# Kernel optimization log

Measured on AMD Instinct MI355X. Metric: run time of the kernel, lower is better.

## Reference

```python
import jax, jax.numpy as jnp
import numpy as np

EPS = 1e-5  # BatchNorm1d eps (eval mode: running_mean=0, running_var=1)

def _bn(h, gamma, beta):
    return h * (gamma / jnp.sqrt(1.0 + EPS)) + beta

def _edgeconv(x, src, dst, W, b, gamma, beta, n_nodes):
    # PyG EdgeConv: message = nn(concat[x_i, x_j - x_i]), aggr='max' at target i
    xi = x[dst]            # [E, D] target features
    xj = x[src]            # [E, D] source features
    m = jnp.concatenate([xi, xj - xi], axis=-1)  # [E, 2D]
    m = _bn(m @ W + b, gamma, beta)              # per-edge Linear + BN
    h = jax.ops.segment_max(m, dst, num_segments=n_nodes)
    # PyG fills nodes with no incoming edges with 0 for max aggregation
    return jnp.where(jnp.isneginf(h), 0.0, h)

def _mean_pool(h, batch, n_graphs):
    s = jax.ops.segment_sum(h, batch, num_segments=n_graphs)
    cnt = jax.ops.segment_sum(jnp.ones((h.shape[0],), h.dtype), batch, num_segments=n_graphs)
    return s / jnp.maximum(cnt, 1.0)[:, None]

def setup_inputs() -> dict:
    key = jax.random.key(0)
    ks = jax.random.split(key, 12)
    N, E, D, G = 65536, 131072, 1024, 64
    x = jax.random.normal(ks[0], (N, D), dtype=jnp.float32)
    edge_index = jax.random.randint(ks[1], (2, E), 0, N, dtype=jnp.int64)
    batch = jnp.sort(jax.random.randint(ks[2], (N,), 0, G, dtype=jnp.int64))
    sc = 1.0 / np.sqrt(D)
    sc2 = 1.0 / np.sqrt(2 * D)
    W0 = jax.random.uniform(ks[3], (D, D), jnp.float32, -sc, sc)
    b0 = jnp.zeros((D,), jnp.float32)
    g0 = jnp.ones((D,), jnp.float32); be0 = jnp.zeros((D,), jnp.float32)
    W1 = jax.random.uniform(ks[4], (2 * D, D), jnp.float32, -sc2, sc2)
    b1 = jnp.zeros((D,), jnp.float32)
    g1 = jnp.ones((D,), jnp.float32); be1 = jnp.zeros((D,), jnp.float32)
    W2 = jax.random.uniform(ks[5], (2 * D, D), jnp.float32, -sc2, sc2)
    b2 = jnp.zeros((D,), jnp.float32)
    g2 = jnp.ones((D,), jnp.float32); be2 = jnp.zeros((D,), jnp.float32)
    Wr = jax.random.uniform(ks[6], (D, 2), jnp.float32, -sc, sc)
    br = jnp.zeros((2,), jnp.float32)
    return dict(x=x, edge_index=edge_index, batch=batch,
                W0=W0, b0=b0, g0=g0, be0=be0,
                W1=W1, b1=b1, g1=g1, be1=be1,
                W2=W2, b2=b2, g2=g2, be2=be2,
                Wr=Wr, br=br)

def reference(x, edge_index, batch, W0, b0, g0, be0, W1, b1, g1, be1, W2, b2, g2, be2, Wr, br):
    N = x.shape[0]
    G = 64
    src, dst = edge_index[0], edge_index[1]
    # Block 0: node-wise Linear+BN, then mean pool (dropout is identity in eval)
    h0 = _bn(x @ W0 + b0, g0, be0)
    p0 = _mean_pool(h0, batch, G)
    # Blocks 1,2: EdgeConv (gather-concat-MLP-scatterMax), then mean pool
    h1 = _edgeconv(x, src, dst, W1, b1, g1, be1, N)
    p1 = _mean_pool(h1, batch, G)
    h2 = _edgeconv(x, src, dst, W2, b2, g2, be2, N)
    p2 = _mean_pool(h2, batch, G)
    acc = p0 + p1 + p2
    return acc @ Wr + br  # [G, 2]
```

## Files before the change

### kernel.cpp

```cpp
#include <hip/hip_runtime.h>
#include <stdint.h>

#define DD   1024
#define GNUM 64

typedef __attribute__((ext_vector_type(8))) short short8;
typedef __attribute__((ext_vector_type(4))) float f32x4;

__device__ __forceinline__ ushort f2bf(float f) {
    unsigned u = __float_as_uint(f);
    u += 0x7FFFu + ((u >> 16) & 1u);
    return (ushort)(u >> 16);
}
__device__ __forceinline__ float bf2f(ushort h) {
    return __uint_as_float(((unsigned)h) << 16);
}

__device__ __forceinline__ void load_lds16(const void* g, void* l) {
    __builtin_amdgcn_global_load_lds(
        (const __attribute__((address_space(1))) unsigned*)(uintptr_t)g,
        (__attribute__((address_space(3))) unsigned*)(uint32_t)(uintptr_t)l,
        16, 0, 0);
}

__device__ __forceinline__ int lbound(const int* a, int n, int v) {
    int lo = 0, hi = n;
    while (lo < hi) { int m = (lo + hi) >> 1; if (a[m] < v) lo = m + 1; else hi = m; }
    return lo;
}

__global__ __launch_bounds__(256) void zero_kernel(int* __restrict__ p, int n) {
    int i = blockIdx.x * 256 + threadIdx.x;
    if (i < n) p[i] = 0;
}

__global__ __launch_bounds__(256) void degflag_kernel(
    const int* __restrict__ ei, int* __restrict__ deg,
    int* __restrict__ flag, int E)
{
    int e = blockIdx.x * 256 + threadIdx.x;
    if (e < E) {
        atomicAdd(&deg[ei[E + e]], 1);
        flag[ei[e]] = 1;
    }
}

__global__ __launch_bounds__(256) void scanA_kernel(
    const int* __restrict__ deg, const int* __restrict__ flag,
    int* __restrict__ ld, int* __restrict__ lf,
    int* __restrict__ bd, int* __restrict__ bf)
{
    __shared__ int sd[256], sf[256];
    const int b = blockIdx.x, t = threadIdx.x;
    const int i = b * 256 + t;
    const int d = deg[i], f = flag[i];
    sd[t] = d; sf[t] = f;
    __syncthreads();
    for (int ofs = 1; ofs < 256; ofs <<= 1) {
        int vd = (t >= ofs) ? sd[t - ofs] : 0;
        int vf = (t >= ofs) ? sf[t - ofs] : 0;
        __syncthreads();
        sd[t] += vd; sf[t] += vf;
        __syncthreads();
    }
    ld[i] = sd[t] - d;
    lf[i] = sf[t] - f;
    if (t == 255) { bd[b] = sd[255]; bf[b] = sf[255]; }
}

__global__ __launch_bounds__(256) void scanB_kernel(
    const int* __restrict__ bd, const int* __restrict__ bf,
    int* __restrict__ od, int* __restrict__ of_, int* __restrict__ nsrc)
{
    __shared__ int sd[256], sf[256];
    const int t = threadIdx.x;
    const int d = bd[t], f = bf[t];
    sd[t] = d; sf[t] = f;
    __syncthreads();
    for (int ofs = 1; ofs < 256; ofs <<= 1) {
        int vd = (t >= ofs) ? sd[t - ofs] : 0;
        int vf = (t >= ofs) ? sf[t - ofs] : 0;
        __syncthreads();
        sd[t] += vd; sf[t] += vf;
        __syncthreads();
    }
    od[t] = sd[t] - d;
    of_[t] = sf[t] - f;
    if (t == 255) *nsrc = sf[255];
}

__global__ __launch_bounds__(256) void scanC_kernel(
    const int* __restrict__ flag, const int* __restrict__ ld,
    const int* __restrict__ lf, const int* __restrict__ od,
    const int* __restrict__ of_, int* __restrict__ rowptr,
    int* __restrict__ cursor, int* __restrict__ rank,
    int* __restrict__ perm, int N, int E)
{
    const int b = blockIdx.x, t = threadIdx.x;
    const int i = b * 256 + t;
    const int rd = od[b] + ld[i];
    rowptr[i] = rd;
    cursor[i] = rd;
    const int rf = of_[b] + lf[i];
    rank[i] = rf;
    if (flag[i]) perm[rf] = i;
    if (i == N - 1) rowptr[N] = E;
}

__global__ __launch_bounds__(256) void scatter_kernel(
    const int* __restrict__ ei, int* __restrict__ cursor,
    const int* __restrict__ rank, int* __restrict__ col, int E)
{
    int e = blockIdx.x * 256 + threadIdx.x;
    if (e < E) {
        int d = ei[E + e];
        int pos = atomicAdd(&cursor[d], 1);
        col[pos] = rank[ei[e]];
    }
}

__global__ __launch_bounds__(256) void cvtmean_kernel(
    const float* __restrict__ x, const int* __restrict__ batch,
    const int* __restrict__ deg, ushort* __restrict__ xh,
    float* __restrict__ pm, float* __restrict__ pp, int N)
{
    const int b = blockIdx.x;
    const int g = b >> 5, sub = b & 31;
    const int d4 = threadIdx.x * 4;

    const int glo = lbound(batch, N, g);
    const int ghi = lbound(batch, N, g + 1);
    const int len = ghi - glo;
    const int s0 = glo + (len * sub) / 32;
    const int s1 = glo + (len * (sub + 1)) / 32;

    float4 sum = make_float4(0.f, 0.f, 0.f, 0.f);
    float4 sump = make_float4(0.f, 0.f, 0.f, 0.f);
    for (int r = s0; r < s1; ++r) {
        float4 v = *(const float4*)(x + (size_t)r * 1024 + d4);
        sum.x += v.x; sum.y += v.y; sum.z += v.z; sum.w += v.w;
        if (deg[r] > 0) { sump.x += v.x; sump.y += v.y; sump.z += v.z; sump.w += v.w; }
        ushort4 h = make_ushort4(f2bf(v.x), f2bf(v.y), f2bf(v.z), f2bf(v.w));
        *(ushort4*)(xh + (size_t)r * 1024 + d4) = h;
    }
    size_t o = (size_t)(g * 32 + sub) * 1024 + d4;
    *(float4*)(pm + o) = sum;
    *(float4*)(pp + o) = sump;
}

__global__ __launch_bounds__(256) void xbar2_kernel(
    const float* __restrict__ pm, const float* __restrict__ pp,
    const int* __restrict__ batch, float* __restrict__ Xbar,
    float* __restrict__ xsp, int N)
{
    int g = blockIdx.x >> 2;
    int c = ((blockIdx.x & 3) << 8) + threadIdx.x;
    float s = 0.f, sp = 0.f;
    #pragma unroll
    for (int k = 0; k < 32; ++k) {
        s  += pm[(size_t)(g * 32 + k) * 1024 + c];
        sp += pp[(size_t)(g * 32 + k) * 1024 + c];
    }
    int cnt = lbound(batch, N, g + 1) - lbound(batch, N, g);
    if (cnt < 1) cnt = 1;
    Xbar[g * 1024 + c] = s / (float)cnt;
    xsp[g * 1024 + c] = sp;
}

__global__ __launch_bounds__(256) void npos_kernel(
    const int* __restrict__ deg, const int* __restrict__ batch,
    float* __restrict__ npos, int N)
{
    __shared__ int r[256];
    int g = blockIdx.x, t = threadIdx.x;
    int glo = lbound(batch, N, g);
    int ghi = lbound(batch, N, g + 1);
    int c = 0;
    for (int i = glo + t; i < ghi; i += 256) c += (deg[i] > 0) ? 1 : 0;
    r[t] = c;
    __syncthreads();
    for (int s = 128; s > 0; s >>= 1) {
        if (t < s) r[t] += r[t + s];
        __syncthreads();
    }
    if (t == 0) npos[g] = (float)r[0];
}

__global__ __launch_bounds__(256) void wbig_kernel(
    const float* __restrict__ W1, const float* __restrict__ W2,
    const float* __restrict__ g1, const float* __restrict__ g2,
    ushort* __restrict__ Wt)
{
    __shared__ float tile[32][33];
    const float SF = 1.0f / sqrtf(1.0f + 1e-5f);
    int k0 = blockIdx.x * 32, c0 = blockIdx.y * 32;
    int tx = threadIdx.x & 31, ty = threadIdx.x >> 5;
    int sec = c0 >> 10;
    int cl = (c0 & 1023) + tx;
    const float* W  = sec ? W2 : W1;
    const float* gv = sec ? g2 : g1;
    float sc = gv[cl] * SF;
    #pragma unroll
    for (int j = 0; j < 4; ++j) {
        int k = k0 + ty + j * 8;
        tile[ty + j * 8][tx] = W[(size_t)(k + 1024) * 1024 + cl] * sc;
    }
    __syncthreads();
    #pragma unroll
    for (int j = 0; j < 4; ++j) {
        int cc = ty + j * 8;
        Wt[(size_t)(c0 + cc) * 1024 + k0 + tx] = f2bf(tile[tx][cc]);
    }
}

__global__ __launch_bounds__(256) void wfold_kernel(
    const float* __restrict__ W0, const float* __restrict__ g0,
    const float* __restrict__ Wr, float* __restrict__ Wfold)
{
    __shared__ float r0s[256], r1s[256];
    const float SF = 1.0f / sqrtf(1.0f + 1e-5f);
    int k = blockIdx.x, t = threadIdx.x;
    float a0 = 0.f, a1 = 0.f;
    for (int c = t; c < 1024; c += 256) {
        float w = W0[(size_t)k * 1024 + c] * (g0[c] * SF);
        a0 += w * Wr[c * 2];
        a1 += w * Wr[c * 2 + 1];
    }
    r0s[t] = a0; r1s[t] = a1;
    __syncthreads();
    for (int s = 128; s > 0; s >>= 1) {
        if (t < s) { r0s[t] += r0s[t + s]; r1s[t] += r1s[t + s]; }
        __syncthreads();
    }
    if (t == 0) { Wfold[k * 2] = r0s[0]; Wfold[k * 2 + 1] = r1s[0]; }
}

__global__ __launch_bounds__(256) void wufold_kernel(
    const float* __restrict__ W1, const float* __restrict__ W2,
    const float* __restrict__ g1, const float* __restrict__ g2,
    const float* __restrict__ Wr, float* __restrict__ Wufold)
{
    __shared__ float r0s[256], r1s[256];
    const float SF = 1.0f / sqrtf(1.0f + 1e-5f);
    int k = blockIdx.x, t = threadIdx.x;
    float a0 = 0.f, a1 = 0.f;
    for (int c = t; c < 1024; c += 256) {
        float wu = (W1[(size_t)k * 1024 + c] - W1[(size_t)(k + 1024) * 1024 + c]) * (g1[c] * SF)
                 + (W2[(size_t)k * 1024 + c] - W2[(size_t)(k + 1024) * 1024 + c]) * (g2[c] * SF);
        a0 += wu * Wr[c * 2];
        a1 += wu * Wr[c * 2 + 1];
    }
    r0s[t] = a0; r1s[t] = a1;
    __syncthreads();
    for (int s = 128; s > 0; s >>= 1) {
        if (t < s) { r0s[t] += r0s[t + s]; r1s[t] += r1s[t + s]; }
        __syncthreads();
    }
    if (t == 0) { Wufold[k * 2] = r0s[0]; Wufold[k * 2 + 1] = r1s[0]; }
}

__global__ __launch_bounds__(256) void bfold_kernel(
    const float* __restrict__ b1, const float* __restrict__ g1, const float* __restrict__ be1,
    const float* __restrict__ b2, const float* __restrict__ g2, const float* __restrict__ be2,
    const float* __restrict__ Wr, float* __restrict__ bUWr)
{
    __shared__ float r0s[256], r1s[256];
    const float SF = 1.0f / sqrtf(1.0f + 1e-5f);
    int t = threadIdx.x;
    float a0 = 0.f, a1 = 0.f;
    for (int c = t; c < 1024; c += 256) {
        float bu = b1[c] * (g1[c] * SF) + be1[c] + b2[c] * (g2[c] * SF) + be2[c];
        a0 += bu * Wr[c * 2];
        a1 += bu * Wr[c * 2 + 1];
    }
    r0s[t] = a0; r1s[t] = a1;
    __syncthreads();
    for (int s = 128; s > 0; s >>= 1) {
        if (t < s) { r0s[t] += r0s[t + s]; r1s[t] += r1s[t + s]; }
        __syncthreads();
    }
    if (t == 0) { bUWr[0] = r0s[0]; bUWr[1] = r1s[0]; }
}

__global__ __launch_bounds__(512, 2) void gemm8_kernel(
    const ushort* __restrict__ A, const ushort* __restrict__ Bt,
    const int* __restrict__ perm, const int* __restrict__ nsrc,
    ushort* __restrict__ C)
{
    __shared__ __align__(16) ushort SM[65536];
    const int tid  = threadIdx.x;
    const int w    = tid >> 6;
    const int lane = tid & 63;
    const int wr = w >> 2;
    const int wc = w & 3;

    const int bx  = blockIdx.x;
    const int cx  = bx & 7;
    const int idx = bx >> 3;
    const int mt  = (idx >> 3) * 8 + cx;
    const int nt  = idx & 7;
    const int m0 = mt * 256;
    const int n0 = nt * 256;

    const int nsv = *nsrc;
    if (m0 >= nsv) return;

    const int srow = lane >> 3;
    const int csw  = ((lane & 7) ^ srow) << 3;

    const int prow = w * 8 + srow;
    int pr[4];
    #pragma unroll
    for (int z = 0; z < 4; ++z) {
        int r = m0 + z * 64 + prow;
        int p_ = perm[r];
        pr[z] = (r < nsv) ? p_ : 0;
    }

    auto stA = [&](int t, int h) {
        if (t >= 16) return;
        const int c = t & 1;
        const ushort* s0 = A + (size_t)pr[2 * h]     * 1024 + t * 64 + csw;
        const ushort* s1 = A + (size_t)pr[2 * h + 1] * 1024 + t * 64 + csw;
        ushort* d = SM + c * 16384 + h * 8192 + w * 512;
        load_lds16(s0, d);
        load_lds16(s1, d + 4096);
    };
    auto stB = [&](int t, int h) {
        if (t >= 16) return;
        const int c = t & 1;
        const ushort* s = Bt + (size_t)(n0 + h * 128 + w * 8 + srow) * 1024 + t * 64 + csw;
        ushort* d = SM + 32768 + c * 16384 + h * 8192 + w * 512;
        load_lds16(s, d);
        load_lds16(s + (size_t)64 * 1024, d + 4096);
    };

    const int cbk0 = ((lane >> 4) << 4);
    const int cbx2 = (lane & 7) << 4;
    auto rdA = [&](int c, int i, int kk) -> short8 {
        int row = i * 16 + (lane & 15);
        int cb  = (kk * 64 + cbk0) ^ cbx2;
        return *(const short8*)((const char*)SM + (c * 16384 + wr * 8192) * 2 + row * 128 + cb);
    };
    auto rdB = [&](int c, int j, int kk) -> short8 {
        int row = (wc & 1) * 64 + j * 16 + (lane & 15);
        int cb  = (kk * 64 + cbk0) ^ cbx2;
        return *(const short8*)((const char*)SM + 65536 + (c * 16384 + (wc >> 1) * 8192) * 2 + row * 128 + cb);
    };

    f32x4 acc[8][4];
    #pragma unroll
    for (int i = 0; i < 8; ++i)
        #pragma unroll
        for (int j = 0; j < 4; ++j)
            acc[i][j] = (f32x4){0.f, 0.f, 0.f, 0.f};

    short8 afr[4][2], bfr[4][2];

    stA(0, 0); stA(0, 1); stB(0, 0); stB(0, 1); stB(1, 0); stB(1, 1);
    asm volatile("s_waitcnt vmcnt(4)" ::: "memory");
    __builtin_amdgcn_s_barrier();

    for (int t = 0; t < 16; ++t) {
        const int c = t & 1;
        #pragma unroll
        for (int i = 0; i < 4; ++i) { afr[i][0] = rdA(c, i, 0); afr[i][1] = rdA(c, i, 1); }
        #pragma unroll
        for (int j = 0; j < 2; ++j) { bfr[j][0] = rdB(c, j, 0); bfr[j][1] = rdB(c, j, 1); }
        stA(t + 1, 0);
        __builtin_amdgcn_s_barrier();
        __builtin_amdgcn_s_setprio(1);
        #pragma unroll
        for (int i = 0; i < 4; ++i)
            #pragma unroll
            for (int j = 0; j < 2; ++j) {
                acc[i][j] = __builtin_amdgcn_mfma_f32_16x16x32_bf16(bfr[j][0], afr[i][0], acc[i][j], 0, 0, 0);
                acc[i][j] = __builtin_amdgcn_mfma_f32_16x16x32_bf16(bfr[j][1], afr[i][1], acc[i][j], 0, 0, 0);
            }
        __builtin_amdgcn_s_setprio(0);
        __builtin_amdgcn_s_barrier();

        #pragma unroll
        for (int j = 2; j < 4; ++j) { bfr[j][0] = rdB(c, j, 0); bfr[j][1] = rdB(c, j, 1); }
        stA(t + 1, 1);
        __builtin_amdgcn_s_barrier();
        __builtin_amdgcn_s_setprio(1);
        #pragma unroll
        for (int i = 0; i < 4; ++i)
            #pragma unroll
            for (int j = 2; j < 4; ++j) {
                acc[i][j] = __builtin_amdgcn_mfma_f32_16x16x32_bf16(bfr[j][0], afr[i][0], acc[i][j], 0, 0, 0);
                acc[i][j] = __builtin_amdgcn_mfma_f32_16x16x32_bf16(bfr[j][1], afr[i][1], acc[i][j], 0, 0, 0);
            }
        __builtin_amdgcn_s_setprio(0);
        __builtin_amdgcn_s_barrier();

        #pragma unroll
        for (int i = 0; i < 4; ++i) { afr[i][0] = rdA(c, i + 4, 0); afr[i][1] = rdA(c, i + 4, 1); }
        stB(t + 2, 0);
        __builtin_amdgcn_s_barrier();
        __builtin_amdgcn_s_setprio(1);
        #pragma unroll
        for (int i = 0; i < 4; ++i)
            #pragma unroll
            for (int j = 2; j < 4; ++j) {
                acc[i + 4][j] = __builtin_amdgcn_mfma_f32_16x16x32_bf16(bfr[j][0], afr[i][0], acc[i + 4][j], 0, 0, 0);
                acc[i + 4][j] = __builtin_amdgcn_mfma_f32_16x16x32_bf16(bfr[j][1], afr[i][1], acc[i + 4][j], 0, 0, 0);
            }
        __builtin_amdgcn_s_setprio(0);
        __builtin_amdgcn_s_barrier();

        stB(t + 2, 1);
        __builtin_amdgcn_s_barrier();
        __builtin_amdgcn_s_setprio(1);
        #pragma unroll
        for (int i = 0; i < 4; ++i)
            #pragma unroll
            for (int j = 0; j < 2; ++j) {
                acc[i + 4][j] = __builtin_amdgcn_mfma_f32_16x16x32_bf16(bfr[j][0], afr[i][0], acc[i + 4][j], 0, 0, 0);
                acc[i + 4][j] = __builtin_amdgcn_mfma_f32_16x16x32_bf16(bfr[j][1], afr[i][1], acc[i + 4][j], 0, 0, 0);
            }
        __builtin_amdgcn_s_setprio(0);
        if (t < 15) {
            if (t < 14) asm volatile("s_waitcnt vmcnt(4)" ::: "memory");
            else        asm volatile("s_waitcnt vmcnt(0)" ::: "memory");
            __builtin_amdgcn_s_barrier();
        }
    }

    __syncthreads();
    {
        const int mls = wr * 128 + (lane & 15);
        const int nls = wc * 64 + ((lane >> 4) << 2);
        #pragma unroll
        for (int j = 0; j < 4; ++j) {
            const int nl = nls + j * 16;
            #pragma unroll
            for (int i = 0; i < 8; ++i) {
                const int ml = mls + i * 16;
                unsigned lo = (unsigned)f2bf(acc[i][j][0]) |
                              ((unsigned)f2bf(acc[i][j][1]) << 16);
                unsigned hi = (unsigned)f2bf(acc[i][j][2]) |
                              ((unsigned)f2bf(acc[i][j][3]) << 16);
                int u = (ml * 256 + nl) ^ ((ml & 15) << 2);
                *(uint2*)(SM + u) = make_uint2(lo, hi);
            }
        }
    }
    __syncthreads();
    #pragma unroll
    for (int p = 0; p < 32; ++p) {
        const int idx2 = p * 512 + tid;
        const int row = idx2 >> 6;
        const int cu  = (idx2 & 63) * 4;
        int u = (row * 256 + cu) ^ ((row & 15) << 2);
        uint2 v = *(const uint2*)(SM + u);
        *(uint2*)(&C[(size_t)(m0 + row) * 2048 + n0 + cu]) = v;
    }
}

__global__ __launch_bounds__(256) void edgepool_kernel(
    const ushort* __restrict__ C, const int* __restrict__ rowptr,
    const int* __restrict__ colb, const int* __restrict__ batch,
    float* __restrict__ partial, int N)
{
    const int b = blockIdx.x;
    const int g = b >> 4, sub = b & 15;
    const int d8 = threadIdx.x * 8;

    const int glo = lbound(batch, N, g);
    const int ghi = lbound(batch, N, g + 1);
    const int len = ghi - glo;
    const int s0 = glo + (len * sub) / 16;
    const int s1 = glo + (len * (sub + 1)) / 16;

    float vsum[8];
    #pragma unroll
    for (int q = 0; q < 8; ++q) vsum[q] = 0.f;

    int lo = (s0 < s1) ? rowptr[s0] : 0;
    for (int node = s0; node < s1; ++node) {
        int hi = rowptr[node + 1];
        if (hi > lo) {
            float vmax[8];
            #pragma unroll
            for (int q = 0; q < 8; ++q) vmax[q] = -3.4e38f;
            for (int j = lo; j < hi; ++j) {
                int src = colb[j];
                short8 v = *(const short8*)(C + (size_t)src * 2048 + d8);
                #pragma unroll
                for (int q = 0; q < 8; ++q)
                    vmax[q] = fmaxf(vmax[q], bf2f((ushort)v[q]));
            }
            #pragma unroll
            for (int q = 0; q < 8; ++q) vsum[q] += vmax[q];
        }
        lo = hi;
    }
    float* p = partial + (size_t)(g * 16 + sub) * 2048 + d8;
    *(float4*)(p)     = make_float4(vsum[0], vsum[1], vsum[2], vsum[3]);
    *(float4*)(p + 4) = make_float4(vsum[4], vsum[5], vsum[6], vsum[7]);
}

__global__ __launch_bounds__(256) void poolreduce_kernel(
    const float* __restrict__ partial, const int* __restrict__ batch,
    float* __restrict__ acc, int N)
{
    int g = blockIdx.x >> 2;
    int c = ((blockIdx.x & 3) << 8) + threadIdx.x;
    float s = 0.f;
    #pragma unroll
    for (int k = 0; k < 16; ++k) {
        const float* p = partial + (size_t)(g * 16 + k) * 2048;
        s += p[c] + p[c + 1024];
    }
    int cnt = lbound(batch, N, g + 1) - lbound(batch, N, g);
    if (cnt < 1) cnt = 1;
    acc[g * 1024 + c] = s / (float)cnt;
}

__global__ __launch_bounds__(256) void final_kernel(
    const float* __restrict__ acc, const float* __restrict__ Xbar,
    const float* __restrict__ xsp, const float* __restrict__ npos,
    const float* __restrict__ Wfold, const float* __restrict__ Wufold,
    const float* __restrict__ bUWr, const float* __restrict__ Wr,
    const float* __restrict__ b0, const float* __restrict__ g0,
    const float* __restrict__ be0, const float* __restrict__ br,
    const int* __restrict__ batch, float* __restrict__ out, int N)
{
    __shared__ float r0[256], r1[256], r2[256], r3[256];
    const float SF = 1.0f / sqrtf(1.0f + 1e-5f);
    int g = blockIdx.x, t = threadIdx.x;
    float p0 = 0.f, p1 = 0.f, q0 = 0.f, q1 = 0.f;
    for (int c = t; c < 1024; c += 256) {
        float a = acc[g * 1024 + c] + b0[c] * (g0[c] * SF) + be0[c];
        p0 += a * Wr[c * 2];
        p1 += a * Wr[c * 2 + 1];
        float xb = Xbar[g * 1024 + c];
        p0 += xb * Wfold[c * 2];
        p1 += xb * Wfold[c * 2 + 1];
        float xs = xsp[g * 1024 + c];
        q0 += xs * Wufold[c * 2];
        q1 += xs * Wufold[c * 2 + 1];
    }
    r0[t] = p0; r1[t] = p1; r2[t] = q0; r3[t] = q1;
    __syncthreads();
    for (int s = 128; s > 0; s >>= 1) {
        if (t < s) {
            r0[t] += r0[t + s]; r1[t] += r1[t + s];
            r2[t] += r2[t + s]; r3[t] += r3[t + s];
        }
        __syncthreads();
    }
    if (t == 0) {
        int cnt = lbound(batch, N, g + 1) - lbound(batch, N, g);
        if (cnt < 1) cnt = 1;
        float ic = 1.0f / (float)cnt;
        out[g * 2 + 0] = r0[0] + (r2[0] + npos[g] * bUWr[0]) * ic + br[0];
        out[g * 2 + 1] = r1[0] + (r3[0] + npos[g] * bUWr[1]) * ic + br[1];
    }
}

extern "C" void kernel_launch(void* const* d_in, const int* in_sizes, int n_in,
                              void* d_out, int out_size, void* d_ws, size_t ws_size,
                              hipStream_t stream)
{
    const float* x   = (const float*)d_in[0];
    const int*   ei  = (const int*)d_in[1];
    const int* batch = (const int*)d_in[2];
    const float* W0  = (const float*)d_in[3];
    const float* b0  = (const float*)d_in[4];
    const float* g0  = (const float*)d_in[5];
    const float* be0 = (const float*)d_in[6];
    const float* W1  = (const float*)d_in[7];
    const float* b1  = (const float*)d_in[8];
    const float* g1  = (const float*)d_in[9];
    const float* be1 = (const float*)d_in[10];
    const float* W2  = (const float*)d_in[11];
    const float* b2  = (const float*)d_in[12];
    const float* g2  = (const float*)d_in[13];
    const float* be2 = (const float*)d_in[14];
    const float* Wr  = (const float*)d_in[15];
    const float* br  = (const float*)d_in[16];
    float* out = (float*)d_out;

    const int N = in_sizes[2];
    const int E = in_sizes[1] / 2;

    char* ws = (char*)d_ws;
    size_t off = 0;
    auto alloc = [&](size_t bytes) -> void* {
        off = (off + 255) & ~(size_t)255;
        void* p = ws + off;
        off += bytes;
        return p;
    };
    ushort*   xh      = (ushort*)alloc((size_t)N * 1024 * 2);
    ushort*   Wt      = (ushort*)alloc((size_t)2048 * 1024 * 2);
    float*    Xbar    = (float*)alloc(64 * 1024 * 4);
    float*    xsp     = (float*)alloc(64 * 1024 * 4);
    float*    accb    = (float*)alloc(64 * 1024 * 4);
    float*    Wfold   = (float*)alloc(1024 * 2 * 4);
    float*    Wufold  = (float*)alloc(1024 * 2 * 4);
    float*    bUWr    = (float*)alloc(256);
    float*    nposb   = (float*)alloc(64 * 4);
    ushort*   Cbuf    = (ushort*)alloc((size_t)N * 2048 * 2);
    float*    partial = (float*)alloc((size_t)1024 * 2048 * 4);
    float*    pm      = (float*)alloc((size_t)2048 * 1024 * 4);
    float*    pp      = (float*)alloc((size_t)2048 * 1024 * 4);
    int*      deg     = (int*)alloc((size_t)N * 4);
    int*      flag    = (int*)alloc((size_t)N * 4);
    int*      rowptr  = (int*)alloc(((size_t)N + 1) * 4);
    int*      cursor  = (int*)alloc((size_t)N * 4);
    int*      rank    = (int*)alloc((size_t)N * 4);
    int*      perm    = (int*)alloc((size_t)N * 4);
    int*      nsrc    = (int*)alloc(256);
    int*      colb    = (int*)alloc((size_t)E * 4);
    int*      ldv     = (int*)alloc((size_t)N * 4);
    int*      lfv     = (int*)alloc((size_t)N * 4);
    int*      bdv     = (int*)alloc(256 * 4);
    int*      bfv     = (int*)alloc(256 * 4);
    int*      odv     = (int*)alloc(256 * 4);
    int*      ofv     = (int*)alloc(256 * 4);
    (void)ws_size; (void)n_in; (void)out_size;

    zero_kernel<<<(N + 255) / 256, 256, 0, stream>>>(deg, N);
    zero_kernel<<<(N + 255) / 256, 256, 0, stream>>>(flag, N);
    degflag_kernel<<<(E + 255) / 256, 256, 0, stream>>>(ei, deg, flag, E);
    scanA_kernel<<<N / 256, 256, 0, stream>>>(deg, flag, ldv, lfv, bdv, bfv);
    scanB_kernel<<<1, 256, 0, stream>>>(bdv, bfv, odv, ofv, nsrc);
    scanC_kernel<<<N / 256, 256, 0, stream>>>(flag, ldv, lfv, odv, ofv,
                                              rowptr, cursor, rank, perm, N, E);
    scatter_kernel<<<(E + 255) / 256, 256, 0, stream>>>(ei, cursor, rank, colb, E);

    cvtmean_kernel<<<2048, 256, 0, stream>>>(x, batch, deg, xh, pm, pp, N);
    xbar2_kernel<<<256, 256, 0, stream>>>(pm, pp, batch, Xbar, xsp, N);
    npos_kernel<<<64, 256, 0, stream>>>(deg, batch, nposb, N);
    wbig_kernel<<<dim3(32, 64), 256, 0, stream>>>(W1, W2, g1, g2, Wt);
    wfold_kernel<<<1024, 256, 0, stream>>>(W0, g0, Wr, Wfold);
    wufold_kernel<<<1024, 256, 0, stream>>>(W1, W2, g1, g2, Wr, Wufold);
    bfold_kernel<<<1, 256, 0, stream>>>(b1, g1, be1, b2, g2, be2, Wr, bUWr);

    gemm8_kernel<<<2048, 512, 0, stream>>>(xh, Wt, perm, nsrc, Cbuf);
    edgepool_kernel<<<1024, 256, 0, stream>>>(Cbuf, rowptr, colb, batch, partial, N);
    poolreduce_kernel<<<256, 256, 0, stream>>>(partial, batch, accb, N);

    final_kernel<<<64, 256, 0, stream>>>(accb, Xbar, xsp, nposb, Wfold, Wufold,
                                         bUWr, Wr, b0, g0, be0, br, batch, out, N);
}
```

Before: 502.8 us.

## Triple-buffer gathered A tiles in GEMM to prefetch two steps ahead

```diff
diff --git a/kernel.cpp b/kernel.cpp
--- a/kernel.cpp
+++ b/kernel.cpp
@@ -282,12 +282,12 @@
     if (t == 0) { bUWr[0] = r0s[0]; bUWr[1] = r1s[0]; }
 }
 
-__global__ __launch_bounds__(512, 2) void gemm8_kernel(
+__global__ __launch_bounds__(512, 1) void gemm8_kernel(
     const ushort* __restrict__ A, const ushort* __restrict__ Bt,
     const int* __restrict__ perm, const int* __restrict__ nsrc,
     ushort* __restrict__ C)
 {
-    __shared__ __align__(16) ushort SM[65536];
+    __shared__ __align__(16) ushort SM[81920];
     const int tid  = threadIdx.x;
     const int w    = tid >> 6;
     const int lane = tid & 63;
@@ -319,33 +319,33 @@
 
     auto stA = [&](int t, int h) {
         if (t >= 16) return;
-        const int c = t & 1;
+        const int c3 = t % 3;
         const ushort* s0 = A + (size_t)pr[2 * h]     * 1024 + t * 64 + csw;
         const ushort* s1 = A + (size_t)pr[2 * h + 1] * 1024 + t * 64 + csw;
-        ushort* d = SM + c * 16384 + h * 8192 + w * 512;
+        ushort* d = SM + c3 * 16384 + h * 8192 + w * 512;
         load_lds16(s0, d);
         load_lds16(s1, d + 4096);
     };
     auto stB = [&](int t, int h) {
         if (t >= 16) return;
-        const int c = t & 1;
+        const int c2 = t & 1;
         const ushort* s = Bt + (size_t)(n0 + h * 128 + w * 8 + srow) * 1024 + t * 64 + csw;
-        ushort* d = SM + 32768 + c * 16384 + h * 8192 + w * 512;
+        ushort* d = SM + 49152 + c2 * 16384 + h * 8192 + w * 512;
         load_lds16(s, d);
         load_lds16(s + (size_t)64 * 1024, d + 4096);
     };
 
     const int cbk0 = ((lane >> 4) << 4);
     const int cbx2 = (lane & 7) << 4;
-    auto rdA = [&](int c, int i, int kk) -> short8 {
+    auto rdA = [&](int c3, int i, int kk) -> short8 {
         int row = i * 16 + (lane & 15);
         int cb  = (kk * 64 + cbk0) ^ cbx2;
-        return *(const short8*)((const char*)SM + (c * 16384 + wr * 8192) * 2 + row * 128 + cb);
+        return *(const short8*)((const char*)SM + (c3 * 16384 + wr * 8192) * 2 + row * 128 + cb);
     };
-    auto rdB = [&](int c, int j, int kk) -> short8 {
+    auto rdB = [&](int c2, int j, int kk) -> short8 {
         int row = (wc & 1) * 64 + j * 16 + (lane & 15);
         int cb  = (kk * 64 + cbk0) ^ cbx2;
-        return *(const short8*)((const char*)SM + 65536 + (c * 16384 + (wc >> 1) * 8192) * 2 + row * 128 + cb);
+        return *(const short8*)((const char*)SM + 98304 + (c2 * 16384 + (wc >> 1) * 8192) * 2 + row * 128 + cb);
     };
 
     f32x4 acc[8][4];
@@ -357,17 +357,19 @@
 
     short8 afr[4][2], bfr[4][2];
 
-    stA(0, 0); stA(0, 1); stB(0, 0); stB(0, 1); stB(1, 0); stB(1, 1);
-    asm volatile("s_waitcnt vmcnt(4)" ::: "memory");
+    stA(0, 0); stA(0, 1); stB(0, 0); stB(0, 1);
+    stA(1, 0); stA(1, 1); stB(1, 0); stB(1, 1);
+    asm volatile("s_waitcnt vmcnt(8)" ::: "memory");
     __builtin_amdgcn_s_barrier();
 
     for (int t = 0; t < 16; ++t) {
-        const int c = t & 1;
-        #pragma unroll
-        for (int i = 0; i < 4; ++i) { afr[i][0] = rdA(c, i, 0); afr[i][1] = rdA(c, i, 1); }
-        #pragma unroll
-        for (int j = 0; j < 2; ++j) { bfr[j][0] = rdB(c, j, 0); bfr[j][1] = rdB(c, j, 1); }
-        stA(t + 1, 0);
+        const int c3 = t % 3;
+        const int c2 = t & 1;
+        #pragma unroll
+        for (int i = 0; i < 4; ++i) { afr[i][0] = rdA(c3, i, 0); afr[i][1] = rdA(c3, i, 1); }
+        #pragma unroll
+        for (int j = 0; j < 2; ++j) { bfr[j][0] = rdB(c2, j, 0); bfr[j][1] = rdB(c2, j, 1); }
+        stA(t + 2, 0);
         __builtin_amdgcn_s_barrier();
         __builtin_amdgcn_s_setprio(1);
         #pragma unroll
@@ -381,8 +383,8 @@
         __builtin_amdgcn_s_barrier();
 
         #pragma unroll
-        for (int j = 2; j < 4; ++j) { bfr[j][0] = rdB(c, j, 0); bfr[j][1] = rdB(c, j, 1); }
-        stA(t + 1, 1);
+        for (int j = 2; j < 4; ++j) { bfr[j][0] = rdB(c2, j, 0); bfr[j][1] = rdB(c2, j, 1); }
+        stA(t + 2, 1);
         __builtin_amdgcn_s_barrier();
         __builtin_amdgcn_s_setprio(1);
         #pragma unroll
@@ -396,7 +398,7 @@
         __builtin_amdgcn_s_barrier();
 
         #pragma unroll
-        for (int i = 0; i < 4; ++i) { afr[i][0] = rdA(c, i + 4, 0); afr[i][1] = rdA(c, i + 4, 1); }
+        for (int i = 0; i < 4; ++i) { afr[i][0] = rdA(c3, i + 4, 0); afr[i][1] = rdA(c3, i + 4, 1); }
         stB(t + 2, 0);
         __builtin_amdgcn_s_barrier();
         __builtin_amdgcn_s_setprio(1);
@@ -422,7 +424,7 @@
             }
         __builtin_amdgcn_s_setprio(0);
         if (t < 15) {
-            if (t < 14) asm volatile("s_waitcnt vmcnt(4)" ::: "memory");
+            if (t < 14) asm volatile("s_waitcnt vmcnt(8)" ::: "memory");
             else        asm volatile("s_waitcnt vmcnt(0)" ::: "memory");
             __builtin_amdgcn_s_barrier();
         }
```

New measurement: 506.4 us. Within noise of the previous version (+0.7%).
